# Performance work log

Hardware: AMD Instinct MI355X
Metric: run time of the kernel (lower is better)

Reference implementation:

```python
import jax, jax.numpy as jnp
import numpy as np

B, Li, Lo, C, E, H = 256, 512, 128, 16, 128, 256


def setup_inputs() -> dict:
    key = jax.random.key(0)
    ks = jax.random.split(key, 12)
    s = 0.08  # small init scale to keep LSTM gates in a sane range
    return {
        "inputs": jax.random.normal(ks[0], (B, Li, C), jnp.float32),
        "emb_W": jax.random.normal(ks[1], (E, C), jnp.float32) * s,
        "emb_b": jnp.zeros((E,), jnp.float32),
        "enc_Wih": jax.random.normal(ks[2], (4 * H, E), jnp.float32) * s,
        "enc_Whh": jax.random.normal(ks[3], (4 * H, H), jnp.float32) * s,
        "enc_b": jnp.zeros((4 * H,), jnp.float32),  # b_ih + b_hh fused
        "dec_Wih": jax.random.normal(ks[4], (4 * H, E), jnp.float32) * s,
        "dec_Whh": jax.random.normal(ks[5], (4 * H, H), jnp.float32) * s,
        "dec_b": jnp.zeros((4 * H,), jnp.float32),
        "att_W1": jax.random.normal(ks[6], (H, H), jnp.float32) * s,
        "att_W2": jax.random.normal(ks[7], (H, H), jnp.float32) * s,  # n_layers*H = H
        "att_V": jax.random.normal(ks[8], (1, H), jnp.float32) * s,
        "dec_input0": jax.random.uniform(ks[9], (E,), jnp.float32),
    }


def _lstm_cell(x, h, c, Wih, Whh, b):
    # PyTorch gate order: i, f, g, o
    g = x @ Wih.T + h @ Whh.T + b
    i, f, gg, o = jnp.split(g, 4, axis=-1)
    c = jax.nn.sigmoid(f) * c + jax.nn.sigmoid(i) * jnp.tanh(gg)
    h = jax.nn.sigmoid(o) * jnp.tanh(c)
    return h, c


def reference(inputs, emb_W, emb_b, enc_Wih, enc_Whh, enc_b,
              dec_Wih, dec_Whh, dec_b, att_W1, att_W2, att_V, dec_input0):
    Bq = inputs.shape[0]
    emb = inputs @ emb_W.T + emb_b  # [B, Li, E]

    # ---- Encoder LSTM over Li (single layer, unidirectional) ----
    h0 = jnp.zeros((Bq, H), inputs.dtype)
    c0 = jnp.zeros((Bq, H), inputs.dtype)

    def enc_step(carry, x_t):
        h, c = carry
        h, c = _lstm_cell(x_t, h, c, enc_Wih, enc_Whh, enc_b)
        return (h, c), h

    (h_enc, c_enc), enc_hs = jax.lax.scan(enc_step, (h0, c0), emb.transpose(1, 0, 2))
    enc_hiddens = enc_hs.transpose(1, 0, 2)  # [B, Li, H]

    # Precompute W1 @ encoder_hiddens once (same math as per-step W1(enc))
    enc_proj = enc_hiddens @ att_W1.T  # [B, Li, H]

    # ---- Decoder: Lo pointer steps ----
    def dec_step(carry, _):
        h, c, x = carry
        h, c = _lstm_cell(x, h, c, dec_Wih, dec_Whh, dec_b)
        dec_term = h @ att_W2.T  # [B, H]
        scores = jnp.tanh(enc_proj + dec_term[:, None, :]) @ att_V[0]  # [B, Li]
        idx = jnp.argmax(scores, axis=1)  # [B]
        x_next = jnp.take_along_axis(emb, idx[:, None, None], axis=1)[:, 0, :]  # [B, E]
        return (h, c, x_next), (scores, idx)

    x0 = jnp.broadcast_to(dec_input0, (Bq, E))
    _, (all_scores, pointers) = jax.lax.scan(
        dec_step, (h_enc, c_enc, x0), None, length=Lo)
    logits = all_scores.transpose(1, 2, 0)  # [B, Li, Lo]
    return logits, pointers.T  # pointers [B, Lo]
```

## Files before the change

### kernel.cpp

```cpp
#include <hip/hip_runtime.h>
#include <math.h>


typedef float vf4 __attribute__((ext_vector_type(4)));

__device__ __forceinline__ float dot4(vf4 a, vf4 b) {
  return a.x * b.x + a.y * b.y + a.z * b.z + a.w * b.w;
}

__device__ __forceinline__ float tanh_fast(float x) {
  float e = __expf(2.0f * x);
  return 1.0f - 2.0f * __builtin_amdgcn_rcpf(e + 1.0f);
}

#define AL(p) __hip_atomic_load((p), __ATOMIC_RELAXED, __HIP_MEMORY_SCOPE_AGENT)
#define AS(p, v) __hip_atomic_store((p), (v), __ATOMIC_RELAXED, __HIP_MEMORY_SCOPE_AGENT)

__global__ __launch_bounds__(512, 2) void pointer_net_kernel(
    const float* __restrict__ inputs,
    const float* __restrict__ emb_W,
    const float* __restrict__ emb_b,
    const float* __restrict__ eWih,
    const float* __restrict__ eWhh,
    const float* __restrict__ eb,
    const float* __restrict__ dWih,
    const float* __restrict__ dWhh,
    const float* __restrict__ db,
    const float* __restrict__ W1,
    const float* __restrict__ W2,
    const float* __restrict__ Vv,
    const float* __restrict__ d0,
    float* __restrict__ out,
    float* __restrict__ encp,
    float* __restrict__ ring,
    int* __restrict__ hflags,
    unsigned int* __restrict__ pflags)
{
  __shared__ float lds_h[16 * 260];
  __shared__ float lds_part[256 * 68];
  __shared__ float lds_pw[256 * 17];
  __shared__ float lds_wx[2][1024];
  __shared__ float lds_sc[512];
  __shared__ float lds_de[512];

  const int tid = threadIdx.x;
  const int B = blockIdx.x;
  const int bi = ((B & 7) << 1) | (B >> 7);
  const int dj = (B >> 3) & 15;
  const int bl = tid >> 4, dl = tid & 15;
  const int b = (bi << 4) + bl;
  const int d = (dj << 4) + dl;
  const int b_own = (bi << 4) + dj;
  const int lane = tid & 63;
  const int wv = tid >> 6;
  const int sdl = tid & 15, sks = (tid >> 4) & 15, sbh8 = (tid >> 8) << 3;
  const int trow = tid >> 5, tcol = (tid & 31) << 3;

  int* hfg = hflags + (bi << 4);
  unsigned int* pfg = pflags + (bi << 4);
  float* ring_g = ring + ((size_t)bi << 14);

  asm volatile("buffer_inv sc1\n\ts_waitcnt vmcnt(0)" ::: "memory");

  vf4 wreg[16], w1reg[4];
  {
    const int k0 = sks << 4;
#pragma unroll
    for (int g = 0; g < 4; ++g) {
      const float* wr = eWhh + ((size_t)((g << 8) + (dj << 4) + sdl)) * 256 + k0;
#pragma unroll
      for (int q = 0; q < 4; ++q) wreg[(g << 2) + q] = *(const vf4*)(wr + (q << 2));
    }
    const float* w1r = W1 + ((size_t)(dj << 4) + sdl) * 256 + k0;
#pragma unroll
    for (int q = 0; q < 4; ++q) w1reg[q] = *(const vf4*)(w1r + (q << 2));
  }

  for (int idx = tid; idx < 1024; idx += 512) {
    int c = idx >> 6, jj = idx & 63;
    int j = ((jj & 3) << 8) + (dj << 4) + (jj >> 2);
    float se = 0.f, sd = 0.f;
    const float* er = eWih + (size_t)j * 128;
    const float* dr = dWih + (size_t)j * 128;
    for (int e = 0; e < 128; ++e) {
      float ew = emb_W[(e << 4) + c];
      se += er[e] * ew;
      sd += dr[e] * ew;
    }
    lds_wx[0][idx] = se;
    lds_wx[1][idx] = sd;
  }
  float benr[4] = {0, 0, 0, 0}, dber[4] = {0, 0, 0, 0},
        dbemb[4] = {0, 0, 0, 0}, g0r[4] = {0, 0, 0, 0};
  if (tid < 256) {
    for (int g = 0; g < 4; ++g) {
      int j = (g << 8) + d;
      const float* er = eWih + (size_t)j * 128;
      const float* dr = dWih + (size_t)j * 128;
      float s1 = 0.f, s2 = 0.f, s3 = 0.f;
      for (int e = 0; e < 128; ++e) {
        s1 += er[e] * emb_b[e];
        s2 += dr[e] * emb_b[e];
        s3 += dr[e] * d0[e];
      }
      benr[g] = eb[j] + s1;
      dber[g] = db[j];
      dbemb[g] = s2;
      g0r[g] = s3;
    }
  }
  vf4 v4a = *((const vf4*)Vv + lane);
  float c_reg = 0.0f;
  __syncthreads();

#define POLL_H(u)                                                                \
  if (tid < 64) {                                                                \
    const int* fp = hfg + (tid & 15);                                            \
    for (;;) {                                                                   \
      int f;                                                                     \
      asm volatile("global_load_dword %0, %1, off sc0 sc1\n\ts_waitcnt vmcnt(0)" \
                   : "=v"(f) : "v"(fp) : "memory");                              \
      if (__ballot(f >= (u)) == ~0ull) break;                                    \
      __builtin_amdgcn_s_sleep(1);                                               \
    }                                                                            \
  }                                                                              \
  __syncthreads();

#define LOAD_TILE(slot)                                                          \
  {                                                                              \
    float* src = ring_g + ((size_t)(slot) << 12) + (trow << 8) + tcol;           \
    float v[8];                                                                  \
    _Pragma("unroll") for (int i = 0; i < 8; ++i) v[i] = AL(src + i);            \
    float* dst = lds_h + trow * 260 + tcol;                                      \
    _Pragma("unroll") for (int i = 0; i < 8; ++i) dst[i] = v[i];                 \
  }                                                                              \
  __syncthreads();

#define SLICE(do_gates, do_w1)                                                   \
  for (int bb = sbh8; bb < sbh8 + 8; ++bb) {                                     \
    const float* hb = lds_h + bb * 260 + (sks << 4);                             \
    vf4 h0 = *(const vf4*)(hb);                                                  \
    vf4 h1 = *(const vf4*)(hb + 4);                                              \
    vf4 h2 = *(const vf4*)(hb + 8);                                              \
    vf4 h3 = *(const vf4*)(hb + 12);                                             \
    int r = (bb << 4) + sks;                                                     \
    if (do_gates) {                                                              \
      vf4 s;                                                                     \
      s.x = dot4(h0, wreg[0]) + dot4(h1, wreg[1]) + dot4(h2, wreg[2]) +          \
            dot4(h3, wreg[3]);                                                   \
      s.y = dot4(h0, wreg[4]) + dot4(h1, wreg[5]) + dot4(h2, wreg[6]) +          \
            dot4(h3, wreg[7]);                                                   \
      s.z = dot4(h0, wreg[8]) + dot4(h1, wreg[9]) + dot4(h2, wreg[10]) +         \
            dot4(h3, wreg[11]);                                                  \
      s.w = dot4(h0, wreg[12]) + dot4(h1, wreg[13]) + dot4(h2, wreg[14]) +       \
            dot4(h3, wreg[15]);                                                  \
      *(vf4*)(lds_part + r * 68 + (sdl << 2)) = s;                               \
    }                                                                            \
    if (do_w1) {                                                                 \
      lds_pw[r * 17 + sdl] = dot4(h0, w1reg[0]) + dot4(h1, w1reg[1]) +           \
                             dot4(h2, w1reg[2]) + dot4(h3, w1reg[3]);            \
    }                                                                            \
  }

#define RED_GATES(a0, a1, a2, a3)                                                \
  _Pragma("unroll") for (int ks = 0; ks < 16; ++ks) {                            \
    vf4 p = *(const vf4*)(lds_part + ((bl << 4) + ks) * 68 + (dl << 2));         \
    a0 += p.x; a1 += p.y; a2 += p.z; a3 += p.w;                                  \
  }

#define WX_ADD(sel, xp, a0, a1, a2, a3)                                          \
  for (int c = 0; c < 16; c += 4) {                                              \
    vf4 xv = *(const vf4*)((xp) + c);                                            \
    vf4 wx0 = *(const vf4*)(&lds_wx[sel][((c + 0) << 6) + (dl << 2)]);           \
    vf4 wx1 = *(const vf4*)(&lds_wx[sel][((c + 1) << 6) + (dl << 2)]);           \
    vf4 wx2 = *(const vf4*)(&lds_wx[sel][((c + 2) << 6) + (dl << 2)]);           \
    vf4 wx3 = *(const vf4*)(&lds_wx[sel][((c + 3) << 6) + (dl << 2)]);           \
    a0 += xv.x * wx0.x + xv.y * wx1.x + xv.z * wx2.x + xv.w * wx3.x;             \
    a1 += xv.x * wx0.y + xv.y * wx1.y + xv.z * wx2.y + xv.w * wx3.y;             \
    a2 += xv.x * wx0.z + xv.y * wx1.z + xv.z * wx2.z + xv.w * wx3.z;             \
    a3 += xv.x * wx0.w + xv.y * wx1.w + xv.z * wx2.w + xv.w * wx3.w;             \
  }

#define ACT_AND_PUBLISH(a0, a1, a2, a3, slot)                                    \
  {                                                                              \
    float ig = 1.0f / (1.0f + expf(-(a0)));                                      \
    float fg = 1.0f / (1.0f + expf(-(a1)));                                      \
    float gg = tanhf(a2);                                                        \
    float og = 1.0f / (1.0f + expf(-(a3)));                                      \
    c_reg = fg * c_reg + ig * gg;                                                \
    float hn = og * tanhf(c_reg);                                                \
    AS(ring_g + ((size_t)(slot) << 12) + (bl << 8) + d, hn);                     \
  }

  for (int t = 0; t < 512; ++t) {
    float a0 = benr[0], a1 = benr[1], a2 = benr[2], a3 = benr[3];
    if (tid < 256) {
      const float* xp = inputs + (size_t)(((b << 9) + t) << 4);
      WX_ADD(0, xp, a0, a1, a2, a3);
    }
    if (t > 0) {
      POLL_H(t);
      LOAD_TILE(t & 3);
      SLICE(1, 1);
      __syncthreads();
    }
    if (tid < 256) {
      if (t > 0) { RED_GATES(a0, a1, a2, a3); }
      ACT_AND_PUBLISH(a0, a1, a2, a3, (t + 1) & 3);
    }
    asm volatile("s_waitcnt vmcnt(0)" ::: "memory");
    __syncthreads();
    if (tid == 0) AS(hfg + dj, t + 1);
    if (t > 0 && tid < 256) {
      float ev = 0.f;
#pragma unroll
      for (int ks = 0; ks < 16; ++ks) ev += lds_pw[((bl << 4) + ks) * 17 + dl];
      AS(encp + (((size_t)((b << 9) + (t - 1))) << 8) + d, ev);
    }
  }

  POLL_H(512);
  LOAD_TILE(0);
  SLICE(0, 1);
  __syncthreads();
  if (tid < 256) {
    float ev = 0.f;
#pragma unroll
    for (int ks = 0; ks < 16; ++ks) ev += lds_pw[((bl << 4) + ks) * 17 + dl];
    AS(encp + (((size_t)((b << 9) + 511)) << 8) + d, ev);
  }
  {
    const int k0 = sks << 4;
#pragma unroll
    for (int g = 0; g < 4; ++g) {
      const float* wr = dWhh + ((size_t)((g << 8) + (dj << 4) + sdl)) * 256 + k0;
#pragma unroll
      for (int q = 0; q < 4; ++q) wreg[(g << 2) + q] = *(const vf4*)(wr + (q << 2));
    }
  }
  SLICE(1, 0);
  __syncthreads();

  for (int j = 0; j < 128; ++j) {
    const int u = 513 + j;
    if (tid < 256) {
      float a0 = dber[0], a1 = dber[1], a2 = dber[2], a3 = dber[3];
      RED_GATES(a0, a1, a2, a3);
      if (j == 0) {
        a0 += g0r[0]; a1 += g0r[1]; a2 += g0r[2]; a3 += g0r[3];
      } else {
        a0 += dbemb[0]; a1 += dbemb[1]; a2 += dbemb[2]; a3 += dbemb[3];
        unsigned int pf;
        for (;;) {
          pf = AL(pfg + bl);
          if ((pf >> 16) == (unsigned int)(j - 1)) break;
          __builtin_amdgcn_s_sleep(1);
        }
        const float* xp = inputs + (size_t)(((b << 9) + (int)(pf & 0xffff)) << 4);
        WX_ADD(1, xp, a0, a1, a2, a3);
      }
      ACT_AND_PUBLISH(a0, a1, a2, a3, u & 3);
    }
    asm volatile("s_waitcnt vmcnt(0)" ::: "memory");
    __syncthreads();
    if (tid == 0) AS(hfg + dj, u);

    POLL_H(u);
    LOAD_TILE(u & 3);

    {
      const int d2 = tid & 255, hf = tid >> 8;
      const float* hrow = lds_h + dj * 260 + (hf << 7);
      const float* w2r = W2 + (size_t)d2 * 256 + (hf << 7);
      float a = 0.f;
      for (int k = 0; k < 128; k += 4) {
        vf4 h4 = *(const vf4*)(hrow + k);
        vf4 q = *(const vf4*)(w2r + k);
        a += dot4(h4, q);
      }
      lds_de[(hf << 8) + d2] = a;
    }
    __syncthreads();

    {
      vf4 p0 = *((const vf4*)lds_de + lane);
      vf4 p1 = *((const vf4*)(lds_de + 256) + lane);
      vf4 d4; d4.x = p0.x + p1.x; d4.y = p0.y + p1.y;
              d4.z = p0.z + p1.z; d4.w = p0.w + p1.w;
      const vf4* bse = (const vf4*)(encp + ((size_t)b_own << 17));
      vf4 A[8], Bv[8];
#pragma unroll
      for (int jj = 0; jj < 8; ++jj)
        A[jj] = bse[((size_t)(wv + (jj << 3)) << 6) + lane];
      for (int ch = 0; ch < 8; ++ch) {
        if (ch < 7) {
#pragma unroll
          for (int jj = 0; jj < 8; ++jj)
            Bv[jj] = bse[((size_t)(wv + (((ch + 1) * 8 + jj) << 3)) << 6) + lane];
        }
#pragma unroll
        for (int jj = 0; jj < 8; ++jj) {
          int li = wv + (((ch << 3) + jj) << 3);
          vf4 e4 = A[jj];
          float s = v4a.x * tanh_fast(e4.x + d4.x)
                  + v4a.y * tanh_fast(e4.y + d4.y)
                  + v4a.z * tanh_fast(e4.z + d4.z)
                  + v4a.w * tanh_fast(e4.w + d4.w);
#pragma unroll
          for (int off = 32; off; off >>= 1) s += __shfl_down(s, off);
          if (lane == 0) lds_sc[li] = s;
        }
#pragma unroll
        for (int jj = 0; jj < 8; ++jj) A[jj] = Bv[jj];
      }
      __syncthreads();

      __builtin_nontemporal_store(lds_sc[tid],
          &out[(size_t)(((b_own << 9) + tid) << 7) + j]);

      if (tid < 64) {
        float bs = -3.402823466e38f;
        int bix = 0;
        for (int i = 0; i < 8; ++i) {
          int idx = (i << 6) + tid;
          float s = lds_sc[idx];
          if (s > bs || (s == bs && idx < bix)) { bs = s; bix = idx; }
        }
#pragma unroll
        for (int off = 32; off; off >>= 1) {
          float os = __shfl_down(bs, off);
          int oi = __shfl_down(bix, off);
          if (os > bs || (os == bs && oi < bix)) { bs = os; bix = oi; }
        }
        if (tid == 0) {
          AS(pfg + dj, ((unsigned int)j << 16) | (unsigned int)bix);
          __builtin_nontemporal_store((float)bix,
              &out[(size_t)16777216 + (b_own << 7) + j]);
        }
      }
    }

    if (j < 127) {
      SLICE(1, 0);
      __syncthreads();
    }
  }
#undef POLL_H
#undef LOAD_TILE
#undef SLICE
#undef RED_GATES
#undef WX_ADD
#undef ACT_AND_PUBLISH
}

extern "C" void kernel_launch(void* const* d_in, const int* in_sizes, int n_in,
                              void* d_out, int out_size, void* d_ws, size_t ws_size,
                              hipStream_t stream) {
  (void)in_sizes; (void)n_in; (void)out_size;
  const float* inputs = (const float*)d_in[0];
  const float* emb_W  = (const float*)d_in[1];
  const float* emb_b  = (const float*)d_in[2];
  const float* eWih   = (const float*)d_in[3];
  const float* eWhh   = (const float*)d_in[4];
  const float* eb     = (const float*)d_in[5];
  const float* dWih   = (const float*)d_in[6];
  const float* dWhh   = (const float*)d_in[7];
  const float* db     = (const float*)d_in[8];
  const float* W1     = (const float*)d_in[9];
  const float* W2     = (const float*)d_in[10];
  const float* Vv     = (const float*)d_in[11];
  const float* d0     = (const float*)d_in[12];

  float* out = (float*)d_out;
  float* encp   = (float*)d_ws;
  float* ring   = encp + 33554432;
  int*   hflags = (int*)(ring + 262144);
  unsigned int* pflags = (unsigned int*)(hflags + 256);

  size_t need = (size_t)(33554432 + 262144 + 512) * 4;
  if (ws_size < need) return;

  hipLaunchKernelGGL(pointer_net_kernel, dim3(256), dim3(512), 0, stream,
                     inputs, emb_W, emb_b, eWih, eWhh, eb, dWih, dWhh, db,
                     W1, W2, Vv, d0, out, encp, ring, hflags, pflags);
}
```

Before: 7.800 ms.

## Split encoder recurrence into two batch halves with separate flags to overlap sync

The encoder step is split into two half-batch groups (8 rows each), each with its own flag array. Each half is polled, loaded, multiplied and published on its own, so one half's cross-block wait can overlap the other half's compute. Ring tile loads now use wide dwordx4 loads that bypass cache instead of scalar atomics, and the decoder prefetch of encp is hoisted above the W2 projection. The cost is twice as many barriers and flag polls per encoder step, plus a larger flag area in the workspace.

Result: faster. 7.517 ms (-3.6%).

```diff
diff --git a/kernel.cpp b/kernel.cpp
--- a/kernel.cpp
+++ b/kernel.cpp
@@ -13,8 +13,24 @@
   return 1.0f - 2.0f * __builtin_amdgcn_rcpf(e + 1.0f);
 }
 
+__device__ __forceinline__ vf4 ld1_sc1(const vf4* p) {
+  vf4 v;
+  asm volatile("global_load_dwordx4 %0, %1, off sc0 sc1\n\ts_waitcnt vmcnt(0)"
+               : "=v"(v) : "v"(p) : "memory");
+  return v;
+}
+
+__device__ __forceinline__ void ld2_sc1(const vf4* p0, const vf4* p1, vf4& v0, vf4& v1) {
+  asm volatile(
+      "global_load_dwordx4 %0, %2, off sc0 sc1\n\t"
+      "global_load_dwordx4 %1, %3, off sc0 sc1\n\t"
+      "s_waitcnt vmcnt(0)"
+      : "=&v"(v0), "=&v"(v1) : "v"(p0), "v"(p1) : "memory");
+}
+
 #define AL(p) __hip_atomic_load((p), __ATOMIC_RELAXED, __HIP_MEMORY_SCOPE_AGENT)
 #define AS(p, v) __hip_atomic_store((p), (v), __ATOMIC_RELAXED, __HIP_MEMORY_SCOPE_AGENT)
+#define DRAIN() asm volatile("s_waitcnt vmcnt(0)" ::: "memory")
 
 __global__ __launch_bounds__(512, 2) void pointer_net_kernel(
     const float* __restrict__ inputs,
@@ -53,10 +69,12 @@
   const int b_own = (bi << 4) + dj;
   const int lane = tid & 63;
   const int wv = tid >> 6;
-  const int sdl = tid & 15, sks = (tid >> 4) & 15, sbh8 = (tid >> 8) << 3;
-  const int trow = tid >> 5, tcol = (tid & 31) << 3;
-
-  int* hfg = hflags + (bi << 4);
+  const int sdl = tid & 15, sks = (tid >> 4) & 15;
+  const int sb4 = (tid >> 8) << 2;
+  const int sbh8 = (tid >> 8) << 3;
+
+  int* fgA = hflags + (bi << 5);
+  int* fgB = fgA + 16;
   unsigned int* pfg = pflags + (bi << 4);
   float* ring_g = ring + ((size_t)bi << 14);
 
@@ -113,9 +131,9 @@
   float c_reg = 0.0f;
   __syncthreads();
 
-#define POLL_H(u)                                                                \
+#define POLL(fb, u)                                                              \
   if (tid < 64) {                                                                \
-    const int* fp = hfg + (tid & 15);                                            \
+    const int* fp = (fb) + (tid & 15);                                           \
     for (;;) {                                                                   \
       int f;                                                                     \
       asm volatile("global_load_dword %0, %1, off sc0 sc1\n\ts_waitcnt vmcnt(0)" \
@@ -126,25 +144,36 @@
   }                                                                              \
   __syncthreads();
 
-#define LOAD_TILE(slot)                                                          \
+#define LOAD_HALF(slot, half)                                                    \
   {                                                                              \
-    float* src = ring_g + ((size_t)(slot) << 12) + (trow << 8) + tcol;           \
-    float v[8];                                                                  \
-    _Pragma("unroll") for (int i = 0; i < 8; ++i) v[i] = AL(src + i);            \
-    float* dst = lds_h + trow * 260 + tcol;                                      \
-    _Pragma("unroll") for (int i = 0; i < 8; ++i) dst[i] = v[i];                 \
+    int grow = ((half) << 3) + (tid >> 6);                                       \
+    int col = (tid & 63) << 2;                                                   \
+    vf4 v = ld1_sc1((const vf4*)(ring_g + ((size_t)(slot) << 12) + (grow << 8) + col)); \
+    *(vf4*)(lds_h + grow * 260 + col) = v;                                       \
   }                                                                              \
   __syncthreads();
 
-#define SLICE(do_gates, do_w1)                                                   \
-  for (int bb = sbh8; bb < sbh8 + 8; ++bb) {                                     \
-    const float* hb = lds_h + bb * 260 + (sks << 4);                             \
+#define LOAD_FULL(slot)                                                          \
+  {                                                                              \
+    int r0 = tid >> 6, col = (tid & 63) << 2;                                    \
+    const float* base = ring_g + ((size_t)(slot) << 12);                         \
+    vf4 v0, v1;                                                                  \
+    ld2_sc1((const vf4*)(base + (r0 << 8) + col),                                \
+            (const vf4*)(base + ((r0 + 8) << 8) + col), v0, v1);                 \
+    *(vf4*)(lds_h + r0 * 260 + col) = v0;                                        \
+    *(vf4*)(lds_h + (r0 + 8) * 260 + col) = v1;                                  \
+  }                                                                              \
+  __syncthreads();
+
+#define SLICE_BODY(bb, do_g, do_w)                                               \
+  {                                                                              \
+    const float* hb = lds_h + (bb)*260 + (sks << 4);                             \
     vf4 h0 = *(const vf4*)(hb);                                                  \
     vf4 h1 = *(const vf4*)(hb + 4);                                              \
     vf4 h2 = *(const vf4*)(hb + 8);                                              \
     vf4 h3 = *(const vf4*)(hb + 12);                                             \
-    int r = (bb << 4) + sks;                                                     \
-    if (do_gates) {                                                              \
+    int r = ((bb) << 4) + sks;                                                   \
+    if (do_g) {                                                                  \
       vf4 s;                                                                     \
       s.x = dot4(h0, wreg[0]) + dot4(h1, wreg[1]) + dot4(h2, wreg[2]) +          \
             dot4(h3, wreg[3]);                                                   \
@@ -156,11 +185,17 @@
             dot4(h3, wreg[15]);                                                  \
       *(vf4*)(lds_part + r * 68 + (sdl << 2)) = s;                               \
     }                                                                            \
-    if (do_w1) {                                                                 \
+    if (do_w) {                                                                  \
       lds_pw[r * 17 + sdl] = dot4(h0, w1reg[0]) + dot4(h1, w1reg[1]) +           \
                              dot4(h2, w1reg[2]) + dot4(h3, w1reg[3]);            \
     }                                                                            \
   }
+
+#define SLICE_HALF(half, do_g, do_w)                                             \
+  for (int q = 0; q < 4; ++q) SLICE_BODY(((half) << 3) + sb4 + q, do_g, do_w)
+
+#define SLICE_FULL(do_g, do_w)                                                   \
+  for (int q = 0; q < 8; ++q) SLICE_BODY(sbh8 + q, do_g, do_w)
 
 #define RED_GATES(a0, a1, a2, a3)                                                \
   _Pragma("unroll") for (int ks = 0; ks < 16; ++ks) {                            \
@@ -181,7 +216,7 @@
     a3 += xv.x * wx0.w + xv.y * wx1.w + xv.z * wx2.w + xv.w * wx3.w;             \
   }
 
-#define ACT_AND_PUBLISH(a0, a1, a2, a3, slot)                                    \
+#define ACT_PUB(a0, a1, a2, a3, slot)                                            \
   {                                                                              \
     float ig = 1.0f / (1.0f + expf(-(a0)));                                      \
     float fg = 1.0f / (1.0f + expf(-(a1)));                                      \
@@ -192,36 +227,65 @@
     AS(ring_g + ((size_t)(slot) << 12) + (bl << 8) + d, hn);                     \
   }
 
-  for (int t = 0; t < 512; ++t) {
-    float a0 = benr[0], a1 = benr[1], a2 = benr[2], a3 = benr[3];
+  {
     if (tid < 256) {
+      float a0 = benr[0], a1 = benr[1], a2 = benr[2], a3 = benr[3];
+      const float* xp = inputs + (size_t)((b << 9) << 4);
+      WX_ADD(0, xp, a0, a1, a2, a3);
+      ACT_PUB(a0, a1, a2, a3, 1);
+    }
+    DRAIN();
+    __syncthreads();
+    if (tid == 0) { AS(fgA + dj, 1); AS(fgB + dj, 1); }
+  }
+
+  for (int t = 1; t < 512; ++t) {
+    float ax0 = 0.f, ax1 = 0.f, ax2 = 0.f, ax3 = 0.f;
+    if (tid < 256) {
+      ax0 = benr[0]; ax1 = benr[1]; ax2 = benr[2]; ax3 = benr[3];
       const float* xp = inputs + (size_t)(((b << 9) + t) << 4);
-      WX_ADD(0, xp, a0, a1, a2, a3);
-    }
-    if (t > 0) {
-      POLL_H(t);
-      LOAD_TILE(t & 3);
-      SLICE(1, 1);
-      __syncthreads();
-    }
-    if (tid < 256) {
-      if (t > 0) { RED_GATES(a0, a1, a2, a3); }
-      ACT_AND_PUBLISH(a0, a1, a2, a3, (t + 1) & 3);
-    }
-    asm volatile("s_waitcnt vmcnt(0)" ::: "memory");
-    __syncthreads();
-    if (tid == 0) AS(hfg + dj, t + 1);
-    if (t > 0 && tid < 256) {
+      WX_ADD(0, xp, ax0, ax1, ax2, ax3);
+    }
+    POLL(fgA, t);
+    LOAD_HALF(t & 3, 0);
+    SLICE_HALF(0, 1, 1);
+    __syncthreads();
+    if (tid < 128) {
+      RED_GATES(ax0, ax1, ax2, ax3);
+      ACT_PUB(ax0, ax1, ax2, ax3, (t + 1) & 3);
+    }
+    DRAIN();
+    __syncthreads();
+    if (tid == 0) AS(fgA + dj, t + 1);
+    if (tid < 128) {
       float ev = 0.f;
 #pragma unroll
       for (int ks = 0; ks < 16; ++ks) ev += lds_pw[((bl << 4) + ks) * 17 + dl];
       AS(encp + (((size_t)((b << 9) + (t - 1))) << 8) + d, ev);
     }
-  }
-
-  POLL_H(512);
-  LOAD_TILE(0);
-  SLICE(0, 1);
+    POLL(fgB, t);
+    LOAD_HALF(t & 3, 1);
+    SLICE_HALF(1, 1, 1);
+    __syncthreads();
+    if (tid >= 128 && tid < 256) {
+      RED_GATES(ax0, ax1, ax2, ax3);
+      ACT_PUB(ax0, ax1, ax2, ax3, (t + 1) & 3);
+    }
+    DRAIN();
+    __syncthreads();
+    if (tid == 0) AS(fgB + dj, t + 1);
+    if (tid >= 128 && tid < 256) {
+      float ev = 0.f;
+#pragma unroll
+      for (int ks = 0; ks < 16; ++ks) ev += lds_pw[((bl << 4) + ks) * 17 + dl];
+      AS(encp + (((size_t)((b << 9) + (t - 1))) << 8) + d, ev);
+    }
+  }
+
+  POLL(fgA, 512);
+  POLL(fgB, 512);
+  LOAD_FULL(0);
+  SLICE_FULL(0, 1);
   __syncthreads();
   if (tid < 256) {
     float ev = 0.f;
@@ -238,7 +302,7 @@
       for (int q = 0; q < 4; ++q) wreg[(g << 2) + q] = *(const vf4*)(wr + (q << 2));
     }
   }
-  SLICE(1, 0);
+  SLICE_FULL(1, 0);
   __syncthreads();
 
   for (int j = 0; j < 128; ++j) {
@@ -259,14 +323,20 @@
         const float* xp = inputs + (size_t)(((b << 9) + (int)(pf & 0xffff)) << 4);
         WX_ADD(1, xp, a0, a1, a2, a3);
       }
-      ACT_AND_PUBLISH(a0, a1, a2, a3, u & 3);
-    }
-    asm volatile("s_waitcnt vmcnt(0)" ::: "memory");
-    __syncthreads();
-    if (tid == 0) AS(hfg + dj, u);
-
-    POLL_H(u);
-    LOAD_TILE(u & 3);
+      ACT_PUB(a0, a1, a2, a3, u & 3);
+    }
+    DRAIN();
+    __syncthreads();
+    if (tid == 0) AS(fgA + dj, u);
+
+    POLL(fgA, u);
+    LOAD_FULL(u & 3);
+
+    const vf4* bse = (const vf4*)(encp + ((size_t)b_own << 17));
+    vf4 A[8], Bv[8];
+#pragma unroll
+    for (int jj = 0; jj < 8; ++jj)
+      A[jj] = bse[((size_t)(wv + (jj << 3)) << 6) + lane];
 
     {
       const int d2 = tid & 255, hf = tid >> 8;
@@ -287,11 +357,6 @@
       vf4 p1 = *((const vf4*)(lds_de + 256) + lane);
       vf4 d4; d4.x = p0.x + p1.x; d4.y = p0.y + p1.y;
               d4.z = p0.z + p1.z; d4.w = p0.w + p1.w;
-      const vf4* bse = (const vf4*)(encp + ((size_t)b_own << 17));
-      vf4 A[8], Bv[8];
-#pragma unroll
-      for (int jj = 0; jj < 8; ++jj)
-        A[jj] = bse[((size_t)(wv + (jj << 3)) << 6) + lane];
       for (int ch = 0; ch < 8; ++ch) {
         if (ch < 7) {
 #pragma unroll
@@ -341,16 +406,19 @@
     }
 
     if (j < 127) {
-      SLICE(1, 0);
+      SLICE_FULL(1, 0);
       __syncthreads();
     }
   }
-#undef POLL_H
-#undef LOAD_TILE
-#undef SLICE
+#undef POLL
+#undef LOAD_HALF
+#undef LOAD_FULL
+#undef SLICE_BODY
+#undef SLICE_HALF
+#undef SLICE_FULL
 #undef RED_GATES
 #undef WX_ADD
-#undef ACT_AND_PUBLISH
+#undef ACT_PUB
 }
 
 extern "C" void kernel_launch(void* const* d_in, const int* in_sizes, int n_in,
@@ -375,9 +443,9 @@
   float* encp   = (float*)d_ws;
   float* ring   = encp + 33554432;
   int*   hflags = (int*)(ring + 262144);
-  unsigned int* pflags = (unsigned int*)(hflags + 256);
-
-  size_t need = (size_t)(33554432 + 262144 + 512) * 4;
+  unsigned int* pflags = (unsigned int*)(hflags + 512);
+
+  size_t need = (size_t)(33554432 + 262144 + 768) * 4;
   if (ws_size < need) return;
 
   hipLaunchKernelGGL(pointer_net_kernel, dim3(256), dim3(512), 0, stream,
```
